# Performance work log

Hardware: AMD Instinct MI355X
Metric: run time of the kernel (lower is better)

## Reference

```python
import jax, jax.numpy as jnp
import numpy as np

B, S, W, MODES, NUM, NLAYERS = 32, 8192, 128, 16, 8, 4
LG = 8192 + 40 - 1  # szie + len - 1 (Gabor filter length)
PI = float(np.pi)


def setup_inputs() -> dict:
    key = jax.random.key(0)
    ks = jax.random.split(key, 10)
    scale = 1.0 / (W * W)
    return {
        "x": jax.random.normal(ks[0], (B, S, 1), jnp.float32),
        "w1_re": scale * jax.random.uniform(ks[1], (NLAYERS, W, W, MODES), jnp.float32),
        "w1_im": scale * jax.random.uniform(ks[2], (NLAYERS, W, W, MODES), jnp.float32),
        "gamma": jnp.tile(jnp.linspace(0.01, 0.02, NUM, dtype=jnp.float32)[None], (NLAYERS, 1)),
        "fwhm": jnp.tile(jnp.linspace(0.001, 0.002, NUM, dtype=jnp.float32)[None], (NLAYERS, 1)),
        "w2": jax.random.uniform(ks[3], (NLAYERS, NUM), jnp.float32),
        "cw": jax.random.normal(ks[4], (NLAYERS, W, W), jnp.float32) / np.sqrt(W),
        "cb": jnp.zeros((NLAYERS, W), jnp.float32),
        "fc0_w": jax.random.normal(ks[5], (W, 2), jnp.float32) / np.sqrt(2.0),
        "fc0_b": jnp.zeros((W,), jnp.float32),
        "fc1_w": jax.random.normal(ks[6], (128, W), jnp.float32) / np.sqrt(W),
        "fc1_b": jnp.zeros((128,), jnp.float32),
        "fc2_w": jax.random.normal(ks[7], (1, 128), jnp.float32) / np.sqrt(128.0),
        "fc2_b": jnp.zeros((1,), jnp.float32),
    }


def _spectral_conv(h, w_re, w_im, gamma, fwhm, w2):
    # h: [B, C, S] real. w_re/w_im: [C, C, MODES]. gamma/fwhm/w2: [NUM].
    u = jnp.linspace(-0.5, 0.5, LG, dtype=h.dtype)                      # [LG]
    t1 = (gamma * PI / (fwhm + 1e-5))[:, None]                          # [NUM,1]
    gab = jnp.exp(-(t1 ** 2) * (u[None, :] - fwhm[:, None]) ** 2)       # [NUM,LG]
    gab = jnp.fft.ifftshift(gab, axes=-1)[:, :MODES]                     # [NUM,MODES]
    # weights2 is a scalar per latent kernel -> fold the num-reduction into an
    # effective per-mode Gabor weight (exact same math as the repeated einsum + sum).
    g_eff = jnp.einsum("k,km->m", w2, gab)                               # [MODES]
    w1 = (w_re + 1j * w_im) * g_eff[None, None, :]                       # [C,C,MODES] complex
    xf = jnp.fft.rfft(h)                                                 # [B,C,F], F=S//2+1
    out_m = jnp.einsum("bim,iom->bom", xf[..., :MODES], w1)              # [B,C,MODES]
    out = jnp.zeros(xf.shape, dtype=xf.dtype).at[..., :MODES].set(out_m)
    return jnp.fft.irfft(out, n=h.shape[-1])                             # [B,C,S]


def reference(x, w1_re, w1_im, gamma, fwhm, w2, cw, cb, fc0_w, fc0_b, fc1_w, fc1_b, fc2_w, fc2_b):
    b, s, _ = x.shape
    grid = jnp.broadcast_to(jnp.linspace(0.0, 1.0, s, dtype=x.dtype)[None, :, None], (b, s, 1))
    h = jnp.concatenate([x, grid], axis=-1)                              # [B,S,2]
    h = h @ fc0_w.T + fc0_b                                              # [B,S,W]
    h = jnp.transpose(h, (0, 2, 1))                                      # [B,W,S]
    for l in range(NLAYERS):
        x1 = _spectral_conv(h, w1_re[l], w1_im[l], gamma[l], fwhm[l], w2[l])
        x2 = jnp.einsum("oi,bis->bos", cw[l], h) + cb[l][None, :, None]  # 1x1 conv
        h = x1 + x2
        if l < NLAYERS - 1:
            h = jax.nn.gelu(h, approximate=False)
    h = jnp.transpose(h, (0, 2, 1))                                      # [B,S,W]
    h = jax.nn.gelu(h @ fc1_w.T + fc1_b, approximate=False)              # [B,S,128]
    return h @ fc2_w.T + fc2_b                                           # [B,S,1]
```

## Files before the change

### kernel.cpp

```cpp
#include <hip/hip_runtime.h>
#include <hip/hip_fp16.h>

#define BB 32
#define SS 8192
#define CC 128
#define MM 16
#define NUMK 8
#define NL 4

#define TWO_PI 6.2831853071795864769f

typedef _Float16 f16x8 __attribute__((ext_vector_type(8)));
typedef float f32x4 __attribute__((ext_vector_type(4)));

#define MFMA16(a, b, c) __builtin_amdgcn_mfma_f32_16x16x32_f16((a), (b), (c), 0, 0, 0)

__device__ __forceinline__ float gelu_f(float v) {
    float u = 0.7978845608f * fmaf(0.044715f * v * v, v, v);
    float a = fabsf(u);
    float e = __expf(-2.0f * a);
    float th = __fdividef(1.0f - e, 1.0f + e);
    th = copysignf(th, u);
    return 0.5f * v * (1.0f + th);
}

__device__ __align__(256) __half g_trigA[SS * 32];
__device__ __align__(256) __half g_trigD[32 * SS];
__device__ __align__(256) __half g_cwh[NL * CC * CC];
__device__ __align__(256) __half g_fc1h[CC * CC];
__device__ __align__(256) __half g_omh[BB * CC * 32];
__device__ __align__(256) float  g_Xfp[BB * 64 * 32 * CC];
__device__ __align__(256) float  g_Xf[BB * 32 * CC];
__device__ __align__(256) float  g_Xx[BB * MM * 2];
__device__ __align__(256) float  g_Xg[MM * 2];

__global__ __launch_bounds__(256) void k_prep(const float* __restrict__ cw,
                                              const float* __restrict__ fc1_w) {
    int idx = blockIdx.x * 256 + threadIdx.x;
    if (idx < NL * CC * CC) g_cwh[idx] = __float2half(cw[idx]);
    if (idx < CC * CC)      g_fc1h[idx] = __float2half(fc1_w[idx]);
}

__global__ __launch_bounds__(256) void k_trig() {
    int s = blockIdx.x * 256 + threadIdx.x;
    for (int m = 0; m < MM; m++) {
        int ms = (m * s) & (SS - 1);
        float th = (float)ms * (TWO_PI / (float)SS);
        float sn, cs;
        sincosf(th, &sn, &cs);
        g_trigA[s * 32 + m]        = __float2half(cs);
        g_trigA[s * 32 + 16 + m]   = __float2half(sn);
        g_trigD[m * SS + s]        = __float2half(cs);
        g_trigD[(16 + m) * SS + s] = __float2half(-sn);
    }
}

__global__ __launch_bounds__(256) void k_dftx(const float* __restrict__ x) {
    __shared__ float red[4][MM][2];
    int blk = blockIdx.x;
    int t = threadIdx.x;
    int lane = t & 63;
    int wv = t >> 6;

    float accR[MM], accI[MM], cr[MM], ci[MM], pc[MM], ps[MM];
#pragma unroll
    for (int m = 0; m < MM; m++) {
        float sn, cs;
        sincosf((TWO_PI / (float)SS) * (float)(m * t), &sn, &cs);
        cr[m] = cs; ci[m] = -sn;
        sincosf((TWO_PI * 256.0f / (float)SS) * (float)m, &sn, &cs);
        pc[m] = cs; ps[m] = -sn;
        accR[m] = 0.f; accI[m] = 0.f;
    }
    for (int k = 0; k < 32; k++) {
        int s = t + (k << 8);
        float v = (blk < BB) ? x[(blk << 13) + s] : (float)s * (1.0f / 8191.0f);
#pragma unroll
        for (int m = 0; m < MM; m++) {
            accR[m] = fmaf(v, cr[m], accR[m]);
            accI[m] = fmaf(v, ci[m], accI[m]);
            float nc = cr[m] * pc[m] - ci[m] * ps[m];
            float ns = cr[m] * ps[m] + ci[m] * pc[m];
            cr[m] = nc; ci[m] = ns;
        }
    }
#pragma unroll
    for (int m = 0; m < MM; m++) {
#pragma unroll
        for (int off = 32; off > 0; off >>= 1) {
            accR[m] += __shfl_xor(accR[m], off, 64);
            accI[m] += __shfl_xor(accI[m], off, 64);
        }
        if (lane == 0) { red[wv][m][0] = accR[m]; red[wv][m][1] = accI[m]; }
    }
    __syncthreads();
    if (t < MM * 2) {
        int m = t >> 1, p = t & 1;
        float s = red[0][m][p] + red[1][m][p] + red[2][m][p] + red[3][m][p];
        if (blk < BB) g_Xx[(blk << 5) + (m << 1) + p] = s;
        else          g_Xg[(m << 1) + p] = s;
    }
}

__global__ __launch_bounds__(256) void k_xf0(const float* __restrict__ fc0_w,
                                             const float* __restrict__ fc0_b) {
    int n = blockIdx.x * 256 + threadIdx.x;
    int i = n & 127, m2 = (n >> 7) & 31, b = n >> 12;
    int m = m2 & 15, p = m2 >> 4;
    float xv = g_Xx[(b << 5) + (m << 1) + p];
    float gv = g_Xg[(m << 1) + p];
    float v = fc0_w[2 * i] * xv + fc0_w[2 * i + 1] * gv;
    if (p == 0 && m == 0) v += (float)SS * fc0_b[i];
    g_Xf[(b << 12) + (m2 << 7) + i] = v;
}

__global__ __launch_bounds__(256) void k_fc0(const float* __restrict__ x,
                                             const float* __restrict__ fc0_w,
                                             const float* __restrict__ fc0_b,
                                             __half2* __restrict__ h2) {
    int idx = blockIdx.x * 256 + threadIdx.x;
    int w2i = idx & 63;
    int s = (idx >> 6) & (SS - 1);
    int b = idx >> 19;
    int w = w2i * 2;
    float g = (float)s * (1.0f / (float)(SS - 1));
    float xv = x[(b << 13) + s];
    float v0 = fmaf(fc0_w[2 * w], xv, fmaf(fc0_w[2 * w + 1], g, fc0_b[w]));
    float v1 = fmaf(fc0_w[2 * w + 2], xv, fmaf(fc0_w[2 * w + 3], g, fc0_b[w + 1]));
    h2[idx] = __floats2half2_rn(v0, v1);
}

__global__ __launch_bounds__(256) void k_red2() {
    int n = blockIdx.x * 256 + threadIdx.x;
    int i = n & 127, m2 = (n >> 7) & 31, b = n >> 12;
    const float* p = g_Xfp + (((b << 6) << 5) + (m2 << 7)) + i;
    float s = 0.f;
#pragma unroll 8
    for (int t = 0; t < 64; t++) s += p[t << 12];
    g_Xf[(b << 12) + (m2 << 7) + i] = s;
}

__global__ __launch_bounds__(256) void k_mix(const float* __restrict__ w1_re,
                                             const float* __restrict__ w1_im,
                                             const float* __restrict__ gamma,
                                             const float* __restrict__ fwhm,
                                             const float* __restrict__ w2,
                                             const float* __restrict__ cb, int l) {
    __shared__ float geff[MM];
    int t = threadIdx.x;
    if (t < MM) {
        float g = 0.f;
        for (int k = 0; k < NUMK; k++) {
            float fw = fwhm[l * NUMK + k];
            float t1 = gamma[l * NUMK + k] * 3.14159265358979f / (fw + 1e-5f);
            float u = (float)t * (1.0f / 8230.0f) - fw;
            g = fmaf(w2[l * NUMK + k], expf(-t1 * t1 * u * u), g);
        }
        geff[t] = g;
    }
    __syncthreads();

    int n = blockIdx.x * 256 + t;
    int m = n & 15, o = (n >> 4) & 127, b = n >> 11;
    const float* xr = g_Xf + (b << 12) + (m << 7);
    const float* xi = g_Xf + (b << 12) + ((16 + m) << 7);
    const float* wr = w1_re + (l << 18) + (o << 4) + m;
    const float* wi = w1_im + (l << 18) + (o << 4) + m;
    float orr = 0.f, oii = 0.f;
    for (int i = 0; i < CC; i++) {
        float xrv = xr[i], xiv = xi[i];
        float wrv = wr[i << 11], wiv = wi[i << 11];
        orr = fmaf(xrv, wrv, orr); orr = fmaf(-xiv, wiv, orr);
        oii = fmaf(xrv, wiv, oii); oii = fmaf(xiv, wrv, oii);
    }
    float sc = geff[m] * (2.0f / (float)SS) * ((m == 0) ? 0.5f : 1.0f);
    float base = (m == 0) ? cb[l * CC + o] : 0.0f;
    g_omh[(b << 12) + (o << 5) + m]      = __float2half(orr * sc + base);
    g_omh[(b << 12) + (o << 5) + 16 + m] = __float2half(-oii * sc);
}

#define GEMM_STEP(KS, HA, HB)                                                       \
    _Pragma("unroll")                                                               \
    for (int af = 0; af < 8; af++) {                                                \
        int row = (af << 4) + lr;                                                   \
        const f16x8 av = *(const f16x8*)(ldsA + (row << 8) +                        \
                          ((((KS << 2) + lg) ^ (row & 7)) << 4));                   \
        acc[af][0] = MFMA16(av, HA, acc[af][0]);                                    \
        acc[af][1] = MFMA16(av, HB, acc[af][1]);                                    \
    }

#define LOAD_HF(S0X)                                                                \
    {                                                                               \
        int hr = (((b << 13) + (S0X) + (wid << 5) + lr) << 8) + (lg << 4);          \
        hf0 = *(const f16x8*)(h_c + hr);                                            \
        hf1 = *(const f16x8*)(h_c + hr + (16 << 8));                                \
        hf2 = *(const f16x8*)(h_c + hr + (1 << 6));                                 \
        hf3 = *(const f16x8*)(h_c + hr + (16 << 8) + (1 << 6));                     \
        hf4 = *(const f16x8*)(h_c + hr + (2 << 6));                                 \
        hf5 = *(const f16x8*)(h_c + hr + (16 << 8) + (2 << 6));                     \
        hf6 = *(const f16x8*)(h_c + hr + (3 << 6));                                 \
        hf7 = *(const f16x8*)(h_c + hr + (16 << 8) + (3 << 6));                     \
        int tr2 = (((S0X) + (wid << 5) + lr) << 6) + (lg << 4);                     \
        tf0 = *(const f16x8*)(ta_c + tr2);                                          \
        tf1 = *(const f16x8*)(ta_c + tr2 + (16 << 6));                              \
    }

template <int TAIL>
__global__ __launch_bounds__(256) void k_layer(__half* __restrict__ h, int l) {
    __shared__ __align__(16) char smem[TAIL ? 73728 : 40960];
    char* ldsA = smem;
    char* ldsO = smem + 32768;
    char* ldsS = smem + (TAIL ? 40960 : 0);
    int bi = blockIdx.x;
    int b = bi >> 4, grp = bi & 15;
    int Sg = grp << 9;
    int t = threadIdx.x;
    int wid = __builtin_amdgcn_readfirstlane(t >> 6);
    int l6 = t & 63, lr = l6 & 15, lg = l6 >> 4;
    const char* h_c = (const char*)h;
    char* hw = (char*)h;
    const char* cw_c = (const char*)(g_cwh + l * CC * CC);
    const char* om_c = (const char*)(g_omh + (b << 12));
    const char* ta_c = (const char*)g_trigA;
    const char* td_c = (const char*)g_trigD;

#pragma unroll
    for (int k = 0; k < 8; k++) {
        int c = (k << 8) + t;
        f16x8 v = *(const f16x8*)(cw_c + (c << 4));
        int row = c >> 4, c16 = c & 15;
        *(f16x8*)(ldsA + (row << 8) + ((c16 ^ (row & 7)) << 4)) = v;
    }
#pragma unroll
    for (int k = 0; k < 2; k++) {
        int c = (k << 8) + t;
        f16x8 v = *(const f16x8*)(om_c + (c << 4));
        int row = c >> 2, c4 = c & 3;
        *(f16x8*)(ldsO + (row << 6) + ((c4 ^ (row & 3)) << 4)) = v;
    }
    f16x8 hf0, hf1, hf2, hf3, hf4, hf5, hf6, hf7, tf0, tf1;
    LOAD_HF(Sg)
    __syncthreads();

    for (int ti = 0; ti < 4; ti++) {
        int S0 = Sg + (ti << 7);
        f32x4 acc[8][2];
#pragma unroll
        for (int af = 0; af < 8; af++) {
            acc[af][0] = (f32x4){0.f, 0.f, 0.f, 0.f};
            acc[af][1] = (f32x4){0.f, 0.f, 0.f, 0.f};
        }
        GEMM_STEP(0, hf0, hf1)
        GEMM_STEP(1, hf2, hf3)
        GEMM_STEP(2, hf4, hf5)
        GEMM_STEP(3, hf6, hf7)
#pragma unroll
        for (int af = 0; af < 8; af++) {
            int row = (af << 4) + lr;
            const f16x8 ov = *(const f16x8*)(ldsO + (row << 6) + ((lg ^ (row & 3)) << 4));
            acc[af][0] = MFMA16(ov, tf0, acc[af][0]);
            acc[af][1] = MFMA16(ov, tf1, acc[af][1]);
        }
        {
            int tn = (ti < 3) ? ti + 1 : ti;
            int S0n = Sg + (tn << 7);
            LOAD_HF(S0n)
        }
#pragma unroll
        for (int bf = 0; bf < 2; bf++) {
            int s_loc = (wid << 5) + (bf << 4) + lr;
            int s = S0 + s_loc;
#pragma unroll
            for (int af = 0; af < 8; af++) {
                int o0 = (af << 4) + (lg << 2);
                float v0 = acc[af][bf][0], v1 = acc[af][bf][1];
                float v2 = acc[af][bf][2], v3 = acc[af][bf][3];
                if (TAIL) { v0 = gelu_f(v0); v1 = gelu_f(v1); v2 = gelu_f(v2); v3 = gelu_f(v3); }
                union { __half2 q[2]; unsigned long long u; } pk;
                pk.q[0] = __floats2half2_rn(v0, v1);
                pk.q[1] = __floats2half2_rn(v2, v3);
                *(unsigned long long*)(hw + (((b << 13) + s) << 8) + (o0 << 1)) = pk.u;
                if (TAIL) {
                    int byte = (s_loc << 8) + ((o0 << 1) ^ ((s_loc & 15) << 4));
                    *(unsigned long long*)(ldsS + byte) = pk.u;
                }
            }
        }
        if (TAIL) {
            __syncthreads();
            f32x4 dacc[2][2];
            dacc[0][0] = (f32x4){0.f, 0.f, 0.f, 0.f};
            dacc[0][1] = (f32x4){0.f, 0.f, 0.f, 0.f};
            dacc[1][0] = (f32x4){0.f, 0.f, 0.f, 0.f};
            dacc[1][1] = (f32x4){0.f, 0.f, 0.f, 0.f};
#pragma unroll
            for (int ks = 0; ks < 4; ks++) {
                int sg = S0 + (ks << 5) + (lg << 3);
                f16x8 a0 = *(const f16x8*)(td_c + (((lr << 13) + sg) << 1));
                f16x8 a1 = *(const f16x8*)(td_c + ((((16 + lr) << 13) + sg) << 1));
                int sl0 = (ks << 5) + (lg << 3);
#pragma unroll
                for (int ogi = 0; ogi < 2; ogi++) {
                    int o = (((wid << 1) + ogi) << 4) + lr;
                    union { unsigned int u[4]; f16x8 v; } bb;
#pragma unroll
                    for (int p = 0; p < 4; p++) {
                        int s0 = sl0 + 2 * p, s1 = s0 + 1;
                        unsigned int lo = *(const unsigned short*)
                            (ldsS + (s0 << 8) + ((o << 1) ^ ((s0 & 15) << 4)));
                        unsigned int hi = *(const unsigned short*)
                            (ldsS + (s1 << 8) + ((o << 1) ^ ((s1 & 15) << 4)));
                        bb.u[p] = lo | (hi << 16);
                    }
                    dacc[ogi][0] = MFMA16(a0, bb.v, dacc[ogi][0]);
                    dacc[ogi][1] = MFMA16(a1, bb.v, dacc[ogi][1]);
                }
            }
            float* xp = g_Xfp + (((b << 6) + (grp << 2) + ti) << 12);
#pragma unroll
            for (int ogi = 0; ogi < 2; ogi++) {
                int o = (((wid << 1) + ogi) << 4) + lr;
#pragma unroll
                for (int mf = 0; mf < 2; mf++)
#pragma unroll
                    for (int reg = 0; reg < 4; reg++) {
                        int m2 = (mf << 4) + (lg << 2) + reg;
                        xp[(m2 << 7) + o] = dacc[ogi][mf][reg];
                    }
            }
            __syncthreads();
        }
    }
}

__global__ __launch_bounds__(256) void k_head(const __half* __restrict__ h,
                                              const float* __restrict__ fc1_b,
                                              const float* __restrict__ fc2_w,
                                              const float* __restrict__ fc2_b,
                                              float* __restrict__ out) {
    __shared__ __align__(16) char smem[32768];
    char* ldsA = smem;
    int bi = blockIdx.x;
    int b = bi >> 4, grp = bi & 15;
    int Sg = grp << 9;
    int t = threadIdx.x;
    int wid = __builtin_amdgcn_readfirstlane(t >> 6);
    int l6 = t & 63, lr = l6 & 15, lg = l6 >> 4;
    const char* h_c = (const char*)h;
    const char* f1_c = (const char*)g_fc1h;
    const char* ta_c = (const char*)g_trigA;

#pragma unroll
    for (int k = 0; k < 8; k++) {
        int c = (k << 8) + t;
        f16x8 v = *(const f16x8*)(f1_c + (c << 4));
        int row = c >> 4, c16 = c & 15;
        *(f16x8*)(ldsA + (row << 8) + ((c16 ^ (row & 7)) << 4)) = v;
    }
    f16x8 hf0, hf1, hf2, hf3, hf4, hf5, hf6, hf7, tf0, tf1;
    LOAD_HF(Sg)
    __syncthreads();

    float f2b = fc2_b[0];
    for (int ti = 0; ti < 4; ti++) {
        int S0 = Sg + (ti << 7);
        f32x4 acc[8][2];
#pragma unroll
        for (int af = 0; af < 8; af++) {
            acc[af][0] = (f32x4){0.f, 0.f, 0.f, 0.f};
            acc[af][1] = (f32x4){0.f, 0.f, 0.f, 0.f};
        }
        GEMM_STEP(0, hf0, hf1)
        GEMM_STEP(1, hf2, hf3)
        GEMM_STEP(2, hf4, hf5)
        GEMM_STEP(3, hf6, hf7)
        {
            int tn = (ti < 3) ? ti + 1 : ti;
            int S0n = Sg + (tn << 7);
            LOAD_HF(S0n)
        }
        float p[2] = {0.f, 0.f};
#pragma unroll
        for (int af = 0; af < 8; af++) {
            float4 fb = *(const float4*)(fc1_b + (af << 4) + (lg << 2));
            float4 f2 = *(const float4*)(fc2_w + (af << 4) + (lg << 2));
#pragma unroll
            for (int bf = 0; bf < 2; bf++) {
                float v0 = gelu_f(acc[af][bf][0] + fb.x);
                float v1 = gelu_f(acc[af][bf][1] + fb.y);
                float v2 = gelu_f(acc[af][bf][2] + fb.z);
                float v3 = gelu_f(acc[af][bf][3] + fb.w);
                p[bf] += f2.x * v0 + f2.y * v1 + f2.z * v2 + f2.w * v3;
            }
        }
#pragma unroll
        for (int bf = 0; bf < 2; bf++) {
            float v = p[bf];
            v += __shfl_xor(v, 16, 64);
            v += __shfl_xor(v, 32, 64);
            if (lg == 0) out[(b << 13) + S0 + (wid << 5) + (bf << 4) + lr] = v + f2b;
        }
    }
}

extern "C" void kernel_launch(void* const* d_in, const int* in_sizes, int n_in,
                              void* d_out, int out_size, void* d_ws, size_t ws_size,
                              hipStream_t stream) {
    const float* x      = (const float*)d_in[0];
    const float* w1_re  = (const float*)d_in[1];
    const float* w1_im  = (const float*)d_in[2];
    const float* gamma  = (const float*)d_in[3];
    const float* fwhm   = (const float*)d_in[4];
    const float* w2     = (const float*)d_in[5];
    const float* cw     = (const float*)d_in[6];
    const float* cb     = (const float*)d_in[7];
    const float* fc0_w  = (const float*)d_in[8];
    const float* fc0_b  = (const float*)d_in[9];
    const float* fc1_w  = (const float*)d_in[10];
    const float* fc1_b  = (const float*)d_in[11];
    const float* fc2_w  = (const float*)d_in[12];
    const float* fc2_b  = (const float*)d_in[13];
    float* out = (float*)d_out;

    __half* h = (__half*)d_ws;

    k_prep<<<dim3(256), dim3(256), 0, stream>>>(cw, fc1_w);
    k_trig<<<dim3(32), dim3(256), 0, stream>>>();
    k_dftx<<<dim3(33), dim3(256), 0, stream>>>(x);
    k_xf0<<<dim3(512), dim3(256), 0, stream>>>(fc0_w, fc0_b);
    k_fc0<<<dim3(65536), dim3(256), 0, stream>>>(x, fc0_w, fc0_b, (__half2*)h);
    for (int l = 0; l < NL; l++) {
        k_mix<<<dim3(256), dim3(256), 0, stream>>>(w1_re, w1_im, gamma, fwhm, w2, cb, l);
        if (l < NL - 1) {
            k_layer<1><<<dim3(512), dim3(256), 0, stream>>>(h, l);
            k_red2<<<dim3(512), dim3(256), 0, stream>>>();
        } else {
            k_layer<0><<<dim3(512), dim3(256), 0, stream>>>(h, l);
        }
    }
    k_head<<<dim3(512), dim3(256), 0, stream>>>(h, fc1_b, fc2_w, fc2_b, out);
}
```

Measured before the change: 372.0 us.

## Make TAIL forward-DFT per-wave with register accumulators, drop block barriers

Restructures the TAIL path so each wave projects only its own 32-sample strip onto the truncated Fourier modes. Partial sums accumulate in registers across all four tiles and are written once at the end, so the two __syncthreads per tile go away and per-tile global writes of partial spectra become one write per wave. It also moves the trig-table loads out of the prefetch macro into the GEMM step, adds s_setprio around the MFMA blocks, and raises launch bounds to ask for two blocks per CU. The costs are many more accumulator registers (dacc grows to 8x2), which may cause spills under the tighter launch bound, and partial spectra indexed per wave rather than per tile, which the downstream reducer must handle consistently.

```diff
diff --git a/kernel.cpp b/kernel.cpp
--- a/kernel.cpp
+++ b/kernel.cpp
@@ -200,13 +200,10 @@
         hf5 = *(const f16x8*)(h_c + hr + (16 << 8) + (2 << 6));                     \
         hf6 = *(const f16x8*)(h_c + hr + (3 << 6));                                 \
         hf7 = *(const f16x8*)(h_c + hr + (16 << 8) + (3 << 6));                     \
-        int tr2 = (((S0X) + (wid << 5) + lr) << 6) + (lg << 4);                     \
-        tf0 = *(const f16x8*)(ta_c + tr2);                                          \
-        tf1 = *(const f16x8*)(ta_c + tr2 + (16 << 6));                              \
     }
 
 template <int TAIL>
-__global__ __launch_bounds__(256) void k_layer(__half* __restrict__ h, int l) {
+__global__ __launch_bounds__(256, 2) void k_layer(__half* __restrict__ h, int l) {
     __shared__ __align__(16) char smem[TAIL ? 73728 : 40960];
     char* ldsA = smem;
     char* ldsO = smem + 32768;
@@ -223,6 +220,7 @@
     const char* om_c = (const char*)(g_omh + (b << 12));
     const char* ta_c = (const char*)g_trigA;
     const char* td_c = (const char*)g_trigD;
+    char* strip = ldsS + (wid << 13);
 
 #pragma unroll
     for (int k = 0; k < 8; k++) {
@@ -238,9 +236,18 @@
         int row = c >> 2, c4 = c & 3;
         *(f16x8*)(ldsO + (row << 6) + ((c4 ^ (row & 3)) << 4)) = v;
     }
-    f16x8 hf0, hf1, hf2, hf3, hf4, hf5, hf6, hf7, tf0, tf1;
+    f16x8 hf0, hf1, hf2, hf3, hf4, hf5, hf6, hf7;
     LOAD_HF(Sg)
     __syncthreads();
+
+    f32x4 dacc[8][2];
+    if (TAIL) {
+#pragma unroll
+        for (int af = 0; af < 8; af++) {
+            dacc[af][0] = (f32x4){0.f, 0.f, 0.f, 0.f};
+            dacc[af][1] = (f32x4){0.f, 0.f, 0.f, 0.f};
+        }
+    }
 
     for (int ti = 0; ti < 4; ti++) {
         int S0 = Sg + (ti << 7);
@@ -250,17 +257,24 @@
             acc[af][0] = (f32x4){0.f, 0.f, 0.f, 0.f};
             acc[af][1] = (f32x4){0.f, 0.f, 0.f, 0.f};
         }
+        __builtin_amdgcn_s_setprio(1);
         GEMM_STEP(0, hf0, hf1)
         GEMM_STEP(1, hf2, hf3)
         GEMM_STEP(2, hf4, hf5)
         GEMM_STEP(3, hf6, hf7)
-#pragma unroll
-        for (int af = 0; af < 8; af++) {
-            int row = (af << 4) + lr;
-            const f16x8 ov = *(const f16x8*)(ldsO + (row << 6) + ((lg ^ (row & 3)) << 4));
-            acc[af][0] = MFMA16(ov, tf0, acc[af][0]);
-            acc[af][1] = MFMA16(ov, tf1, acc[af][1]);
-        }
+        {
+            int tr2 = ((S0 + (wid << 5) + lr) << 6) + (lg << 4);
+            f16x8 tf0 = *(const f16x8*)(ta_c + tr2);
+            f16x8 tf1 = *(const f16x8*)(ta_c + tr2 + (16 << 6));
+#pragma unroll
+            for (int af = 0; af < 8; af++) {
+                int row = (af << 4) + lr;
+                const f16x8 ov = *(const f16x8*)(ldsO + (row << 6) + ((lg ^ (row & 3)) << 4));
+                acc[af][0] = MFMA16(ov, tf0, acc[af][0]);
+                acc[af][1] = MFMA16(ov, tf1, acc[af][1]);
+            }
+        }
+        __builtin_amdgcn_s_setprio(0);
         {
             int tn = (ti < 3) ? ti + 1 : ti;
             int S0n = Sg + (tn << 7);
@@ -268,8 +282,8 @@
         }
 #pragma unroll
         for (int bf = 0; bf < 2; bf++) {
-            int s_loc = (wid << 5) + (bf << 4) + lr;
-            int s = S0 + s_loc;
+            int s_w = (bf << 4) + lr;
+            int s = S0 + (wid << 5) + s_w;
 #pragma unroll
             for (int af = 0; af < 8; af++) {
                 int o0 = (af << 4) + (lg << 2);
@@ -281,55 +295,47 @@
                 pk.q[1] = __floats2half2_rn(v2, v3);
                 *(unsigned long long*)(hw + (((b << 13) + s) << 8) + (o0 << 1)) = pk.u;
                 if (TAIL) {
-                    int byte = (s_loc << 8) + ((o0 << 1) ^ ((s_loc & 15) << 4));
-                    *(unsigned long long*)(ldsS + byte) = pk.u;
+                    int byte = (s_w << 8) + ((o0 << 1) ^ ((s_w & 15) << 4));
+                    *(unsigned long long*)(strip + byte) = pk.u;
                 }
             }
         }
         if (TAIL) {
-            __syncthreads();
-            f32x4 dacc[2][2];
-            dacc[0][0] = (f32x4){0.f, 0.f, 0.f, 0.f};
-            dacc[0][1] = (f32x4){0.f, 0.f, 0.f, 0.f};
-            dacc[1][0] = (f32x4){0.f, 0.f, 0.f, 0.f};
-            dacc[1][1] = (f32x4){0.f, 0.f, 0.f, 0.f};
-#pragma unroll
-            for (int ks = 0; ks < 4; ks++) {
-                int sg = S0 + (ks << 5) + (lg << 3);
-                f16x8 a0 = *(const f16x8*)(td_c + (((lr << 13) + sg) << 1));
-                f16x8 a1 = *(const f16x8*)(td_c + ((((16 + lr) << 13) + sg) << 1));
-                int sl0 = (ks << 5) + (lg << 3);
-#pragma unroll
-                for (int ogi = 0; ogi < 2; ogi++) {
-                    int o = (((wid << 1) + ogi) << 4) + lr;
-                    union { unsigned int u[4]; f16x8 v; } bb;
-#pragma unroll
-                    for (int p = 0; p < 4; p++) {
-                        int s0 = sl0 + 2 * p, s1 = s0 + 1;
-                        unsigned int lo = *(const unsigned short*)
-                            (ldsS + (s0 << 8) + ((o << 1) ^ ((s0 & 15) << 4)));
-                        unsigned int hi = *(const unsigned short*)
-                            (ldsS + (s1 << 8) + ((o << 1) ^ ((s1 & 15) << 4)));
-                        bb.u[p] = lo | (hi << 16);
-                    }
-                    dacc[ogi][0] = MFMA16(a0, bb.v, dacc[ogi][0]);
-                    dacc[ogi][1] = MFMA16(a1, bb.v, dacc[ogi][1]);
+            asm volatile("s_waitcnt lgkmcnt(0)" ::: "memory");
+            __builtin_amdgcn_sched_barrier(0);
+            int sgl = S0 + (wid << 5) + (lg << 3);
+            f16x8 a0 = *(const f16x8*)(td_c + (((lr << 13) + sgl) << 1));
+            f16x8 a1 = *(const f16x8*)(td_c + ((((16 + lr) << 13) + sgl) << 1));
+#pragma unroll
+            for (int af = 0; af < 8; af++) {
+                int o = (af << 4) + lr;
+                union { unsigned int u[4]; f16x8 v; } bb;
+#pragma unroll
+                for (int p = 0; p < 4; p++) {
+                    int s0 = (lg << 3) + 2 * p, s1 = s0 + 1;
+                    unsigned int lo = *(const unsigned short*)
+                        (strip + (s0 << 8) + ((o << 1) ^ ((s0 & 15) << 4)));
+                    unsigned int hi = *(const unsigned short*)
+                        (strip + (s1 << 8) + ((o << 1) ^ ((s1 & 15) << 4)));
+                    bb.u[p] = lo | (hi << 16);
                 }
+                dacc[af][0] = MFMA16(a0, bb.v, dacc[af][0]);
+                dacc[af][1] = MFMA16(a1, bb.v, dacc[af][1]);
             }
-            float* xp = g_Xfp + (((b << 6) + (grp << 2) + ti) << 12);
-#pragma unroll
-            for (int ogi = 0; ogi < 2; ogi++) {
-                int o = (((wid << 1) + ogi) << 4) + lr;
-#pragma unroll
-                for (int mf = 0; mf < 2; mf++)
-#pragma unroll
-                    for (int reg = 0; reg < 4; reg++) {
-                        int m2 = (mf << 4) + (lg << 2) + reg;
-                        xp[(m2 << 7) + o] = dacc[ogi][mf][reg];
-                    }
-            }
-            __syncthreads();
-        }
+        }
+    }
+    if (TAIL) {
+        float* xp = g_Xfp + (((b << 6) + (grp << 2) + wid) << 12);
+#pragma unroll
+        for (int af = 0; af < 8; af++)
+#pragma unroll
+            for (int mh = 0; mh < 2; mh++)
+#pragma unroll
+                for (int reg = 0; reg < 4; reg++) {
+                    int m2 = (mh << 4) + (lg << 2) + reg;
+                    int o = (af << 4) + lr;
+                    xp[(m2 << 7) + o] = dacc[af][mh][reg];
+                }
     }
 }
 
@@ -348,7 +354,6 @@
     int l6 = t & 63, lr = l6 & 15, lg = l6 >> 4;
     const char* h_c = (const char*)h;
     const char* f1_c = (const char*)g_fc1h;
-    const char* ta_c = (const char*)g_trigA;
 
 #pragma unroll
     for (int k = 0; k < 8; k++) {
@@ -357,7 +362,7 @@
         int row = c >> 4, c16 = c & 15;
         *(f16x8*)(ldsA + (row << 8) + ((c16 ^ (row & 7)) << 4)) = v;
     }
-    f16x8 hf0, hf1, hf2, hf3, hf4, hf5, hf6, hf7, tf0, tf1;
+    f16x8 hf0, hf1, hf2, hf3, hf4, hf5, hf6, hf7;
     LOAD_HF(Sg)
     __syncthreads();
 
@@ -370,10 +375,12 @@
             acc[af][0] = (f32x4){0.f, 0.f, 0.f, 0.f};
             acc[af][1] = (f32x4){0.f, 0.f, 0.f, 0.f};
         }
+        __builtin_amdgcn_s_setprio(1);
         GEMM_STEP(0, hf0, hf1)
         GEMM_STEP(1, hf2, hf3)
         GEMM_STEP(2, hf4, hf5)
         GEMM_STEP(3, hf6, hf7)
+        __builtin_amdgcn_s_setprio(0);
         {
             int tn = (ti < 3) ? ti + 1 : ti;
             int S0n = Sg + (tn << 7);
```

New measurement: 344.9 us. 1.08x faster.
